# Kernel tuning notes

Measured on AMD Instinct MI355X. Metric: run time of the kernel, lower is better.

## Reference

```python
import jax, jax.numpy as jnp
import numpy as np
import math

D_MODEL = 512
H = 8
DK = D_MODEL // H  # 64
B, S = 2, 4096


def setup_inputs() -> dict:
    key = jax.random.key(0)
    ks = jax.random.split(key, 11)
    sc = 1.0 / math.sqrt(D_MODEL)
    return {
        "query": jax.random.normal(ks[0], (B, S, D_MODEL), jnp.float32),
        "key": jax.random.normal(ks[1], (B, S, D_MODEL), jnp.float32),
        "value": jax.random.normal(ks[2], (B, S, D_MODEL), jnp.float32),
        "Wq": jax.random.normal(ks[3], (D_MODEL, D_MODEL), jnp.float32) * sc,
        "bq": jnp.zeros((D_MODEL,), jnp.float32),
        "Wk": jax.random.normal(ks[4], (D_MODEL, D_MODEL), jnp.float32) * sc,
        "bk": jnp.zeros((D_MODEL,), jnp.float32),
        "Wv": jax.random.normal(ks[5], (D_MODEL, D_MODEL), jnp.float32) * sc,
        "bv": jnp.zeros((D_MODEL,), jnp.float32),
        "Wo": jax.random.normal(ks[6], (D_MODEL, D_MODEL), jnp.float32) * sc,
        "bo": jnp.zeros((D_MODEL,), jnp.float32),
    }


def reference(query, key, value, Wq, bq, Wk, bk, Wv, bv, Wo, bo):
    b = query.shape[0]
    # projections; W stored [in, out]
    def proj(x, W, bias):
        y = x @ W + bias                      # [B,S,h*dk]
        return y.reshape(b, -1, H, DK).transpose(0, 2, 1, 3)  # [B,h,S,dk]

    q = proj(query, Wq, bq)
    k = proj(key, Wk, bk)
    v = proj(value, Wv, bv)
    scores = jnp.einsum("bhqd,bhkd->bhqk", q, k) / math.sqrt(DK)
    attn = jax.nn.softmax(scores, axis=-1)    # [B,h,Sq,Sk]
    ctx = jnp.einsum("bhqk,bhkd->bhqd", attn, v)
    ctx = ctx.transpose(0, 2, 1, 3).reshape(b, -1, H * DK)  # [B,S,d_model]
    return ctx @ Wo + bo
```

## Files before the change

### kernel.cpp

```cpp
#include <hip/hip_runtime.h>
#include <hip/hip_bf16.h>

#define DM   512
#define HEADS 8
#define DKH  64
#define BATCH 2
#define SEQ  4096

typedef float  f32x4  __attribute__((ext_vector_type(4)));
typedef float  f32x16 __attribute__((ext_vector_type(16)));
typedef __bf16 bf16x8 __attribute__((ext_vector_type(8)));
typedef __bf16 bf16x4 __attribute__((ext_vector_type(4)));
typedef __bf16 bf16x2 __attribute__((ext_vector_type(2)));

static __device__ __forceinline__ f32x4 mfma16(bf16x8 a, bf16x8 b, f32x4 c) {
    return __builtin_amdgcn_mfma_f32_16x16x32_bf16(a, b, c, 0, 0, 0);
}
static __device__ __forceinline__ f32x16 mfma32(bf16x8 a, bf16x8 b, f32x16 c) {
    return __builtin_amdgcn_mfma_f32_32x32x16_bf16(a, b, c, 0, 0, 0);
}

#define GLD16(gp, lp) __builtin_amdgcn_global_load_lds( \
    (const __attribute__((address_space(1))) void*)(gp), \
    (__attribute__((address_space(3))) void*)(lp), 16, 0, 0)

struct Cvt3 { const float* s[3]; __bf16* d[3]; };

__global__ __launch_bounds__(256) void convert_x3(Cvt3 a) {
    const float* s = a.s[blockIdx.y];
    __bf16* d = a.d[blockIdx.y];
    const size_t i = ((size_t)blockIdx.x * 256 + threadIdx.x) * 8;
    f32x4 f0 = *(const f32x4*)&s[i];
    f32x4 f1 = *(const f32x4*)&s[i + 4];
    bf16x8 v;
    v[0] = (__bf16)f0[0]; v[1] = (__bf16)f0[1]; v[2] = (__bf16)f0[2]; v[3] = (__bf16)f0[3];
    v[4] = (__bf16)f1[0]; v[5] = (__bf16)f1[1]; v[6] = (__bf16)f1[2]; v[7] = (__bf16)f1[3];
    *(bf16x8*)&d[i] = v;
}

struct WtAll { const float* W[4]; __bf16* Wt[4]; };

__global__ __launch_bounds__(256) void wt_convert_all(WtAll a) {
    const float* W = a.W[blockIdx.z];
    __bf16* Wt = a.Wt[blockIdx.z];
    __shared__ float tile[32][33];
    const int tx = threadIdx.x & 31, ty = threadIdx.x >> 5;
    const int nb = blockIdx.x * 32, kb = blockIdx.y * 32;
#pragma unroll
    for (int i = 0; i < 4; ++i)
        tile[ty + 8 * i][tx] = W[(size_t)(kb + ty + 8 * i) * DM + nb + tx];
    __syncthreads();
#pragma unroll
    for (int i = 0; i < 4; ++i)
        Wt[(size_t)(nb + ty + 8 * i) * DM + kb + tx] = (__bf16)tile[tx][ty + 8 * i];
}

struct Ptr3 { const void* A; const __bf16* Bt; const float* bias; void* Out; float ascale; };
struct GemmArgs { Ptr3 p[3]; };

template <bool A_FP32, bool OUT_BF16>
__global__ __launch_bounds__(256) void gemm_tile(GemmArgs args) {
    __shared__ __bf16 Al[128][64];
    __shared__ __bf16 Bl[128][64];
    const Ptr3 P = args.p[blockIdx.z];
    const int tid = threadIdx.x;
    const int lane = tid & 63, wid = tid >> 6;
    const int lq = lane & 15, hi = lane >> 4;
    const int m0 = blockIdx.x * 128, n0 = blockIdx.y * 128;
    const int wm = (wid >> 1) * 64, wn = (wid & 1) * 64;

    const int srow = wid * 32 + (lane >> 3);
    const int scol = (lane & 7) * 8;
    const __bf16* gb = P.Bt + (size_t)(n0 + srow) * DM + scol;
    const __bf16* ga = (const __bf16*)P.A + (size_t)(m0 + srow) * DM + scol;

    f32x4 acc[4][4] = {};

    for (int kt = 0; kt < DM / 64; ++kt) {
        const int k0 = kt * 64;
        if (kt) __syncthreads();
        if (A_FP32) {
            const float* A = (const float*)P.A;
            bf16x8 abuf[4];
#pragma unroll
            for (int i = 0; i < 4; ++i) {
                int cc = tid + 256 * i, row = cc >> 3, col = cc & 7;
                const f32x4* src = (const f32x4*)&A[(size_t)(m0 + row) * DM + k0 + col * 8];
                f32x4 f0 = src[0], f1 = src[1];
                bf16x8 v;
                v[0] = (__bf16)f0[0]; v[1] = (__bf16)f0[1]; v[2] = (__bf16)f0[2]; v[3] = (__bf16)f0[3];
                v[4] = (__bf16)f1[0]; v[5] = (__bf16)f1[1]; v[6] = (__bf16)f1[2]; v[7] = (__bf16)f1[3];
                abuf[i] = v;
            }
#pragma unroll
            for (int i = 0; i < 4; ++i) {
                int cc = tid + 256 * i, row = cc >> 3, col = cc & 7;
                *(bf16x8*)&Al[row][col * 8] = abuf[i];
            }
        } else {
#pragma unroll
            for (int i = 0; i < 4; ++i)
                GLD16(ga + k0 + (size_t)i * 8 * DM, &Al[wid * 32 + i * 8][0]);
        }
#pragma unroll
        for (int i = 0; i < 4; ++i)
            GLD16(gb + k0 + (size_t)i * 8 * DM, &Bl[wid * 32 + i * 8][0]);
        __syncthreads();

        __builtin_amdgcn_s_setprio(1);
#pragma unroll
        for (int ks = 0; ks < 2; ++ks) {
            bf16x8 af[4], bfv[4];
#pragma unroll
            for (int i = 0; i < 4; ++i)
                af[i] = *(const bf16x8*)&Al[wm + i * 16 + lq][ks * 32 + hi * 8];
#pragma unroll
            for (int j = 0; j < 4; ++j)
                bfv[j] = *(const bf16x8*)&Bl[wn + j * 16 + lq][ks * 32 + hi * 8];
#pragma unroll
            for (int i = 0; i < 4; ++i)
#pragma unroll
                for (int j = 0; j < 4; ++j)
                    acc[i][j] = mfma16(af[i], bfv[j], acc[i][j]);
        }
        __builtin_amdgcn_s_setprio(0);
    }
    const float* bias = P.bias;
    const float asc = P.ascale;
#pragma unroll
    for (int j = 0; j < 4; ++j) {
        const int n = n0 + wn + j * 16 + lq;
        const float bv = bias[n];
#pragma unroll
        for (int i = 0; i < 4; ++i) {
#pragma unroll
            for (int r = 0; r < 4; ++r) {
                const int m = m0 + wm + i * 16 + hi * 4 + r;
                const float v = (acc[i][j][r] + bv) * asc;
                if (OUT_BF16) ((__bf16*)P.Out)[(size_t)m * DM + n] = (__bf16)v;
                else          ((float*)P.Out)[(size_t)m * DM + n] = v;
            }
        }
    }
}

__global__ __launch_bounds__(256) void v_transpose(const __bf16* __restrict__ Vp,
                                                   __bf16* __restrict__ Vt) {
    __shared__ __bf16 tile[64][72];
    const int tid = threadIdx.x;
    const int tt = blockIdx.x * 64;
    const int bh = blockIdx.y, b = bh >> 3, h = bh & 7;
#pragma unroll
    for (int i = 0; i < 2; ++i) {
        int c = tid + 256 * i, row = c >> 3, cc = c & 7;
        *(bf16x8*)&tile[row][cc * 8] =
            *(const bf16x8*)&Vp[(size_t)(b * SEQ + tt + row) * DM + h * DKH + cc * 8];
    }
    __syncthreads();
#pragma unroll
    for (int i = 0; i < 2; ++i) {
        int c = tid + 256 * i, row = c >> 3, cc = c & 7;
        bf16x8 v;
#pragma unroll
        for (int j = 0; j < 8; ++j) v[j] = tile[cc * 8 + j][row];
        *(bf16x8*)&Vt[(size_t)(bh * DKH + row) * SEQ + tt + cc * 8] = v;
    }
}

template <bool SPLIT>
__global__ __launch_bounds__(256, 4) void flash_attn3(const __bf16* __restrict__ Qp,
                                                      const __bf16* __restrict__ Kp,
                                                      const __bf16* __restrict__ Vt,
                                                      __bf16* __restrict__ O0,
                                                      __bf16* __restrict__ O1,
                                                      float2* __restrict__ ml) {
    __shared__ __bf16 Kl[2][64][64];
    __shared__ __bf16 Vl[2][64][64];
    __shared__ float  Lbuf[4][32];

    const int tid = threadIdx.x, lane = tid & 63, w = tid >> 6;
    const int c = lane & 31, h = lane >> 5;
    const int bh = blockIdx.y, b = bh >> 3, hd = bh & 7;
    const int qbase = blockIdx.x * 128 + w * 32;
    const int kvoff = SPLIT ? blockIdx.z * (SEQ / 2) : 0;
    const int NT = SPLIT ? (SEQ / 2) / 64 : SEQ / 64;

    bf16x8 qf[4];
#pragma unroll
    for (int t = 0; t < 4; ++t)
        qf[t] = *(const bf16x8*)&Qp[(size_t)(b * SEQ + qbase + c) * DM + hd * DKH + 16 * t + 8 * h];

    const int r0 = w * 16 + (lane >> 3);
    const int r1 = r0 + 8;
    const int s0 = (lane & 7) ^ ((r0 ^ (r0 >> 3)) & 7);
    const int s1 = (lane & 7) ^ ((r1 ^ (r1 >> 3)) & 7);
    const __bf16* kg0 = Kp + (size_t)(b * SEQ + kvoff + r0) * DM + hd * DKH + s0 * 8;
    const __bf16* kg1 = Kp + (size_t)(b * SEQ + kvoff + r1) * DM + hd * DKH + s1 * 8;
    const __bf16* vg0 = Vt + (size_t)(bh * DKH + r0) * SEQ + kvoff + s0 * 8;
    const __bf16* vg1 = Vt + (size_t)(bh * DKH + r1) * SEQ + kvoff + s1 * 8;

    const int swz0 = (c ^ (c >> 3)) & 7;
    const int swz1 = ((32 + c) ^ ((32 + c) >> 3)) & 7;
    const int rowb0 = c * 128, rowb1 = (32 + c) * 128;
    const char* kb = (const char*)&Kl[0][0][0];
    const char* vb = (const char*)&Vl[0][0][0];

    f32x16 acc0 = {}, acc1 = {};
    float m_run = -__builtin_inff(), l_run = 0.f;

    GLD16(kg0, &Kl[0][w * 16][0]);
    GLD16(kg1, &Kl[0][w * 16 + 8][0]);
    GLD16(vg0, &Vl[0][w * 16][0]);
    GLD16(vg1, &Vl[0][w * 16 + 8][0]);
    __syncthreads();

    for (int kvt = 0; kvt < NT; ++kvt) {
        const int cur = kvt & 1;
        if (kvt + 1 < NT) {
            const size_t ko = (size_t)(kvt + 1) * 64 * DM;
            const size_t vo = (size_t)(kvt + 1) * 64;
            GLD16(kg0 + ko, &Kl[cur ^ 1][w * 16][0]);
            GLD16(kg1 + ko, &Kl[cur ^ 1][w * 16 + 8][0]);
            GLD16(vg0 + vo, &Vl[cur ^ 1][w * 16][0]);
            GLD16(vg1 + vo, &Vl[cur ^ 1][w * 16 + 8][0]);
        }
        const char* kc = kb + cur * (64 * 128);
        const char* vc = vb + cur * (64 * 128);

        f32x16 sa = {}, sb = {};
        __builtin_amdgcn_s_setprio(1);
#pragma unroll
        for (int t = 0; t < 4; ++t) {
            bf16x8 kf0 = *(const bf16x8*)(kc + rowb0 + (((2 * t + h) ^ swz0) << 4));
            sa = mfma32(kf0, qf[t], sa);
            bf16x8 kf1 = *(const bf16x8*)(kc + rowb1 + (((2 * t + h) ^ swz1) << 4));
            sb = mfma32(kf1, qf[t], sb);
        }
        __builtin_amdgcn_s_setprio(0);

        float mx = sa[0];
#pragma unroll
        for (int r = 1; r < 16; ++r) mx = fmaxf(mx, sa[r]);
#pragma unroll
        for (int r = 0; r < 16; ++r) mx = fmaxf(mx, sb[r]);
        mx = fmaxf(mx, __shfl_xor(mx, 32));
        if (!__all(mx <= m_run + 8.f)) {
            const float mnew = fmaxf(m_run, mx);
            const float al = __builtin_amdgcn_exp2f(m_run - mnew);
            m_run = mnew;
            l_run *= al;
            if (lane < 32) Lbuf[w][lane] = al;
#pragma unroll
            for (int r = 0; r < 16; ++r) {
                const float a2 = Lbuf[w][(r & 3) + 8 * (r >> 2) + 4 * h];
                acc0[r] *= a2; acc1[r] *= a2;
            }
        }
        float ls = 0.f;
        float pa[16], pb[16];
#pragma unroll
        for (int r = 0; r < 16; ++r) { pa[r] = __builtin_amdgcn_exp2f(sa[r] - m_run); ls += pa[r]; }
#pragma unroll
        for (int r = 0; r < 16; ++r) { pb[r] = __builtin_amdgcn_exp2f(sb[r] - m_run); ls += pb[r]; }
        ls += __shfl_xor(ls, 32);
        l_run += ls;

        int ua[4][2], ub[4][2];
#pragma unroll
        for (int q4 = 0; q4 < 4; ++q4)
#pragma unroll
            for (int i = 0; i < 2; ++i) {
                bf16x2 ta; ta[0] = (__bf16)pa[4 * q4 + 2 * i]; ta[1] = (__bf16)pa[4 * q4 + 2 * i + 1];
                ua[q4][i] = __builtin_bit_cast(int, ta);
                bf16x2 tb; tb[0] = (__bf16)pb[4 * q4 + 2 * i]; tb[1] = (__bf16)pb[4 * q4 + 2 * i + 1];
                ub[q4][i] = __builtin_bit_cast(int, tb);
            }

#pragma unroll
        for (int tg = 0; tg < 4; ++tg) {
            int x0, y0, x1, y1;
            if (tg < 2) {
                x0 = ua[2 * tg][0]; y0 = ua[2 * tg + 1][0];
                x1 = ua[2 * tg][1]; y1 = ua[2 * tg + 1][1];
            } else {
                x0 = ub[2 * (tg - 2)][0]; y0 = ub[2 * (tg - 2) + 1][0];
                x1 = ub[2 * (tg - 2)][1]; y1 = ub[2 * (tg - 2) + 1][1];
            }
            asm("v_permlane32_swap_b32 %0, %1" : "+v"(x0), "+v"(y0));
            asm("v_permlane32_swap_b32 %0, %1" : "+v"(x1), "+v"(y1));
            union { int i4[4]; bf16x8 v; } pf;
            pf.i4[0] = x0; pf.i4[1] = x1; pf.i4[2] = y0; pf.i4[3] = y1;
            bf16x8 vf0 = *(const bf16x8*)(vc + rowb0 + (((2 * tg + h) ^ swz0) << 4));
            bf16x8 vf1 = *(const bf16x8*)(vc + rowb1 + (((2 * tg + h) ^ swz1) << 4));
            __builtin_amdgcn_s_setprio(1);
            acc0 = mfma32(pf.v, vf0, acc0);
            acc1 = mfma32(pf.v, vf1, acc1);
            __builtin_amdgcn_s_setprio(0);
        }
        __syncthreads();
    }

    if (SPLIT) {
        __bf16* pp = blockIdx.z ? O1 : O0;
#pragma unroll
        for (int r = 0; r < 16; ++r) {
            const int qr = (r & 3) + 8 * (r >> 2) + 4 * h;
            const size_t off = (size_t)(b * SEQ + qbase + qr) * DM + hd * DKH;
            pp[off + c]      = (__bf16)acc0[r];
            pp[off + 32 + c] = (__bf16)acc1[r];
        }
        if (h == 0) {
            float2 v; v.x = m_run; v.y = l_run;
            ml[(size_t)(blockIdx.z * 16 + bh) * SEQ + qbase + c] = v;
        }
    } else {
        if (lane < 32) Lbuf[w][lane] = l_run;
        __bf16* outp = O0 + (size_t)(b * SEQ + qbase) * DM + hd * DKH;
#pragma unroll
        for (int r = 0; r < 16; ++r) {
            const int qr = (r & 3) + 8 * (r >> 2) + 4 * h;
            const float li = 1.f / Lbuf[w][qr];
            outp[(size_t)qr * DM + c]      = (__bf16)(acc0[r] * li);
            outp[(size_t)qr * DM + 32 + c] = (__bf16)(acc1[r] * li);
        }
    }
}

__global__ __launch_bounds__(256) void combine(const __bf16* __restrict__ P0,
                                               const __bf16* __restrict__ P1,
                                               const float2* __restrict__ ml,
                                               __bf16* __restrict__ Ctx) {
    const int row = blockIdx.x;
    const int b = row >> 12, q = row & (SEQ - 1);
    const int col = threadIdx.x * 2;
    const int head = col >> 6;
    const int bh = b * HEADS + head;
    const float2 ml0 = ml[(size_t)bh * SEQ + q];
    const float2 ml1 = ml[(size_t)(16 + bh) * SEQ + q];
    const float m = fmaxf(ml0.x, ml1.x);
    const float e0 = __builtin_amdgcn_exp2f(ml0.x - m);
    const float e1 = __builtin_amdgcn_exp2f(ml1.x - m);
    const float inv = 1.f / (ml0.y * e0 + ml1.y * e1);
    const float f0 = e0 * inv, f1 = e1 * inv;
    const size_t idx = (size_t)row * DM + col;
    bf16x2 a = *(const bf16x2*)&P0[idx];
    bf16x2 bb = *(const bf16x2*)&P1[idx];
    bf16x2 o;
    o[0] = (__bf16)((float)a[0] * f0 + (float)bb[0] * f1);
    o[1] = (__bf16)((float)a[1] * f0 + (float)bb[1] * f1);
    *(bf16x2*)&Ctx[idx] = o;
}

extern "C" void kernel_launch(void* const* d_in, const int* in_sizes, int n_in,
                              void* d_out, int out_size, void* d_ws, size_t ws_size,
                              hipStream_t stream) {
    (void)in_sizes; (void)n_in; (void)out_size;
    const float* query = (const float*)d_in[0];
    const float* key_  = (const float*)d_in[1];
    const float* value = (const float*)d_in[2];
    const float* Wq = (const float*)d_in[3];
    const float* bq = (const float*)d_in[4];
    const float* Wk = (const float*)d_in[5];
    const float* bk = (const float*)d_in[6];
    const float* Wv = (const float*)d_in[7];
    const float* bv = (const float*)d_in[8];
    const float* Wo = (const float*)d_in[9];
    const float* bo = (const float*)d_in[10];

    char* ws = (char*)d_ws;
    const size_t WSZ = (size_t)512 * 1024;
    const size_t XSZ = (size_t)8 * 1024 * 1024;
    const float QSC = 0.125f * 1.4426950408889634f;

    __bf16* Wtq = (__bf16*)(ws);
    __bf16* Wtk = (__bf16*)(ws + WSZ);
    __bf16* Wtv = (__bf16*)(ws + 2 * WSZ);
    __bf16* Wto = (__bf16*)(ws + 3 * WSZ);
    char* xb = ws + 4 * WSZ;

    WtAll wa;
    wa.W[0] = Wq; wa.W[1] = Wk; wa.W[2] = Wv; wa.W[3] = Wo;
    wa.Wt[0] = Wtq; wa.Wt[1] = Wtk; wa.Wt[2] = Wtv; wa.Wt[3] = Wto;

    if (ws_size >= 4 * WSZ + 7 * XSZ) {
        __bf16* Qb = (__bf16*)(xb);
        __bf16* Kb = (__bf16*)(xb + XSZ);
        __bf16* Vb = (__bf16*)(xb + 2 * XSZ);
        __bf16* Qp = (__bf16*)(xb + 3 * XSZ);
        __bf16* Kp = (__bf16*)(xb + 4 * XSZ);
        __bf16* Vp = (__bf16*)(xb + 5 * XSZ);
        __bf16* Vt = (__bf16*)(xb + 6 * XSZ);
        __bf16* Ctx = Vp;
        __bf16* P0 = Qb;
        __bf16* P1 = Kb;
        float2* mlp = (float2*)Vb;

        Cvt3 cv;
        cv.s[0] = query; cv.s[1] = key_; cv.s[2] = value;
        cv.d[0] = Qb; cv.d[1] = Kb; cv.d[2] = Vb;
        convert_x3<<<dim3(2048, 3), 256, 0, stream>>>(cv);
        wt_convert_all<<<dim3(16, 16, 4), 256, 0, stream>>>(wa);

        GemmArgs qa;
        qa.p[0] = {Qb, Wtq, bq, Qp, QSC};
        qa.p[1] = {Kb, Wtk, bk, Kp, 1.0f};
        qa.p[2] = {Vb, Wtv, bv, Vp, 1.0f};
        gemm_tile<false, true><<<dim3(64, 4, 3), 256, 0, stream>>>(qa);

        v_transpose<<<dim3(SEQ / 64, BATCH * HEADS), 256, 0, stream>>>(Vp, Vt);

        flash_attn3<true><<<dim3(SEQ / 128, BATCH * HEADS, 2), 256, 0, stream>>>(
            Qp, Kp, Vt, P0, P1, mlp);

        combine<<<dim3(BATCH * SEQ), 256, 0, stream>>>(P0, P1, mlp, Ctx);

        GemmArgs oa;
        oa.p[0] = {Ctx, Wto, bo, d_out, 1.0f};
        oa.p[1] = oa.p[0]; oa.p[2] = oa.p[0];
        gemm_tile<false, false><<<dim3(64, 4, 1), 256, 0, stream>>>(oa);
    } else {
        if (ws_size < 4 * WSZ + 4 * XSZ) return;
        __bf16* Qp = (__bf16*)(xb);
        __bf16* Kp = (__bf16*)(xb + XSZ);
        __bf16* Vp = (__bf16*)(xb + 2 * XSZ);
        __bf16* Vt = (__bf16*)(xb + 3 * XSZ);
        __bf16* Ctx = Vp;

        wt_convert_all<<<dim3(16, 16, 4), 256, 0, stream>>>(wa);

        GemmArgs qa;
        qa.p[0] = {query, Wtq, bq, Qp, QSC};
        qa.p[1] = {key_,  Wtk, bk, Kp, 1.0f};
        qa.p[2] = {value, Wtv, bv, Vp, 1.0f};
        gemm_tile<true, true><<<dim3(64, 4, 3), 256, 0, stream>>>(qa);

        v_transpose<<<dim3(SEQ / 64, BATCH * HEADS), 256, 0, stream>>>(Vp, Vt);

        flash_attn3<false><<<dim3(SEQ / 128, BATCH * HEADS, 1), 256, 0, stream>>>(
            Qp, Kp, Vt, Ctx, nullptr, nullptr);

        GemmArgs oa;
        oa.p[0] = {Ctx, Wto, bo, d_out, 1.0f};
        oa.p[1] = oa.p[0]; oa.p[2] = oa.p[0];
        gemm_tile<false, false><<<dim3(64, 4, 1), 256, 0, stream>>>(oa);
    }
}
```

Baseline: 251.4 us.

## Double-buffer GEMM and attention loads, compute row sums via MFMA, swizzle GEMM LDS

The projection GEMM now double-buffers its LDS tiles with explicit vmcnt waits and raw barriers, and uses an XOR-swizzled LDS layout to avoid bank conflicts. The output GEMM switches to a 64-wide N tile so twice as many blocks are launched. The attention kernel issues the loads for tile t+2 after compute, keeping two tiles in flight. It also computes the softmax row sum with an extra MFMA against a ones vector instead of a scalar reduction and cross-lane shuffle. The fallback small-workspace path is removed, and m/l are stored as separate arrays.

```diff
diff --git a/kernel.cpp b/kernel.cpp
--- a/kernel.cpp
+++ b/kernel.cpp
@@ -10,7 +10,6 @@
 typedef float  f32x4  __attribute__((ext_vector_type(4)));
 typedef float  f32x16 __attribute__((ext_vector_type(16)));
 typedef __bf16 bf16x8 __attribute__((ext_vector_type(8)));
-typedef __bf16 bf16x4 __attribute__((ext_vector_type(4)));
 typedef __bf16 bf16x2 __attribute__((ext_vector_type(2)));
 
 static __device__ __forceinline__ f32x4 mfma16(bf16x8 a, bf16x8 b, f32x4 c) {
@@ -23,6 +22,16 @@
 #define GLD16(gp, lp) __builtin_amdgcn_global_load_lds( \
     (const __attribute__((address_space(1))) void*)(gp), \
     (__attribute__((address_space(3))) void*)(lp), 16, 0, 0)
+
+#define WAITVM(n) asm volatile("s_waitcnt vmcnt(" #n ")" ::: "memory")
+
+static __device__ __forceinline__ void barrier_sync() {
+    __builtin_amdgcn_sched_barrier(0);
+    asm volatile("" ::: "memory");
+    __builtin_amdgcn_s_barrier();
+    asm volatile("" ::: "memory");
+    __builtin_amdgcn_sched_barrier(0);
+}
 
 struct Cvt3 { const float* s[3]; __bf16* d[3]; };
 
@@ -55,80 +64,103 @@
         Wt[(size_t)(nb + ty + 8 * i) * DM + kb + tx] = (__bf16)tile[tx][ty + 8 * i];
 }
 
-struct Ptr3 { const void* A; const __bf16* Bt; const float* bias; void* Out; float ascale; };
+struct Ptr3 { const __bf16* A; const __bf16* Bt; const float* bias; void* Out; float ascale; };
 struct GemmArgs { Ptr3 p[3]; };
 
-template <bool A_FP32, bool OUT_BF16>
+template <bool OUT_BF16, int BN>
 __global__ __launch_bounds__(256) void gemm_tile(GemmArgs args) {
-    __shared__ __bf16 Al[128][64];
-    __shared__ __bf16 Bl[128][64];
+    constexpr int BGLD = BN / 32;
+    constexpr int NJ   = BN / 32;
+    constexpr int NT   = DM / 64;
+    __shared__ __bf16 Al[2][128][64];
+    __shared__ __bf16 Bl[2][BN][64];
     const Ptr3 P = args.p[blockIdx.z];
     const int tid = threadIdx.x;
     const int lane = tid & 63, wid = tid >> 6;
     const int lq = lane & 15, hi = lane >> 4;
-    const int m0 = blockIdx.x * 128, n0 = blockIdx.y * 128;
-    const int wm = (wid >> 1) * 64, wn = (wid & 1) * 64;
-
-    const int srow = wid * 32 + (lane >> 3);
-    const int scol = (lane & 7) * 8;
-    const __bf16* gb = P.Bt + (size_t)(n0 + srow) * DM + scol;
-    const __bf16* ga = (const __bf16*)P.A + (size_t)(m0 + srow) * DM + scol;
-
-    f32x4 acc[4][4] = {};
-
-    for (int kt = 0; kt < DM / 64; ++kt) {
+    const int m0 = blockIdx.x * 128, n0 = blockIdx.y * BN;
+    const int wm = (wid >> 1) * 64, wn = (wid & 1) * (BN / 2);
+
+    const int lrow = lane >> 3, lslot = lane & 7;
+    const __bf16* gaP[4];
+#pragma unroll
+    for (int i = 0; i < 4; ++i) {
+        const int r = wid * 32 + i * 8 + lrow;
+        const int s = lslot ^ ((r ^ (r >> 3)) & 7);
+        gaP[i] = P.A + (size_t)(m0 + r) * DM + s * 8;
+    }
+    const __bf16* gbP[BGLD];
+#pragma unroll
+    for (int i = 0; i < BGLD; ++i) {
+        const int r = wid * (BN / 4) + i * 8 + lrow;
+        const int s = lslot ^ ((r ^ (r >> 3)) & 7);
+        gbP[i] = P.Bt + (size_t)(n0 + r) * DM + s * 8;
+    }
+    auto stage = [&](int kt, int buf) {
         const int k0 = kt * 64;
-        if (kt) __syncthreads();
-        if (A_FP32) {
-            const float* A = (const float*)P.A;
-            bf16x8 abuf[4];
-#pragma unroll
-            for (int i = 0; i < 4; ++i) {
-                int cc = tid + 256 * i, row = cc >> 3, col = cc & 7;
-                const f32x4* src = (const f32x4*)&A[(size_t)(m0 + row) * DM + k0 + col * 8];
-                f32x4 f0 = src[0], f1 = src[1];
-                bf16x8 v;
-                v[0] = (__bf16)f0[0]; v[1] = (__bf16)f0[1]; v[2] = (__bf16)f0[2]; v[3] = (__bf16)f0[3];
-                v[4] = (__bf16)f1[0]; v[5] = (__bf16)f1[1]; v[6] = (__bf16)f1[2]; v[7] = (__bf16)f1[3];
-                abuf[i] = v;
-            }
-#pragma unroll
-            for (int i = 0; i < 4; ++i) {
-                int cc = tid + 256 * i, row = cc >> 3, col = cc & 7;
-                *(bf16x8*)&Al[row][col * 8] = abuf[i];
-            }
-        } else {
+#pragma unroll
+        for (int i = 0; i < 4; ++i)
+            GLD16(gaP[i] + k0, &Al[buf][wid * 32 + i * 8][0]);
+#pragma unroll
+        for (int i = 0; i < BGLD; ++i)
+            GLD16(gbP[i] + k0, &Bl[buf][wid * (BN / 4) + i * 8][0]);
+    };
+
+    int baseA[4], swA[4];
+#pragma unroll
+    for (int i = 0; i < 4; ++i) {
+        const int r = wm + i * 16 + lq;
+        baseA[i] = r * 128;
+        swA[i] = (((r ^ (r >> 3)) & 7) << 4);
+    }
+    int baseB[NJ], swB[NJ];
+#pragma unroll
+    for (int j = 0; j < NJ; ++j) {
+        const int r = wn + j * 16 + lq;
+        baseB[j] = r * 128;
+        swB[j] = (((r ^ (r >> 3)) & 7) << 4);
+    }
+
+    f32x4 acc[4][NJ] = {};
+
+    stage(0, 0);
+    stage(1, 1);
+    for (int kt = 0; kt < NT; ++kt) {
+        const int cur = kt & 1;
+        if (kt + 1 < NT) {
+            if (BN == 128) { WAITVM(8); } else { WAITVM(6); }
+        } else { WAITVM(0); }
+        barrier_sync();
+        const char* Ab = (const char*)&Al[cur][0][0];
+        const char* Bb = (const char*)&Bl[cur][0][0];
+        __builtin_amdgcn_s_setprio(1);
+#pragma unroll
+        for (int ks = 0; ks < 2; ++ks) {
+            const int off = ks * 64 + hi * 16;
+            bf16x8 af[4], bfv[NJ];
 #pragma unroll
             for (int i = 0; i < 4; ++i)
-                GLD16(ga + k0 + (size_t)i * 8 * DM, &Al[wid * 32 + i * 8][0]);
-        }
-#pragma unroll
-        for (int i = 0; i < 4; ++i)
-            GLD16(gb + k0 + (size_t)i * 8 * DM, &Bl[wid * 32 + i * 8][0]);
-        __syncthreads();
-
-        __builtin_amdgcn_s_setprio(1);
-#pragma unroll
-        for (int ks = 0; ks < 2; ++ks) {
-            bf16x8 af[4], bfv[4];
+                af[i] = *(const bf16x8*)(Ab + baseA[i] + (off ^ swA[i]));
+#pragma unroll
+            for (int j = 0; j < NJ; ++j)
+                bfv[j] = *(const bf16x8*)(Bb + baseB[j] + (off ^ swB[j]));
 #pragma unroll
             for (int i = 0; i < 4; ++i)
-                af[i] = *(const bf16x8*)&Al[wm + i * 16 + lq][ks * 32 + hi * 8];
-#pragma unroll
-            for (int j = 0; j < 4; ++j)
-                bfv[j] = *(const bf16x8*)&Bl[wn + j * 16 + lq][ks * 32 + hi * 8];
-#pragma unroll
-            for (int i = 0; i < 4; ++i)
-#pragma unroll
-                for (int j = 0; j < 4; ++j)
+#pragma unroll
+                for (int j = 0; j < NJ; ++j)
                     acc[i][j] = mfma16(af[i], bfv[j], acc[i][j]);
         }
         __builtin_amdgcn_s_setprio(0);
-    }
+        if (kt + 2 < NT) {
+            barrier_sync();
+            stage(kt + 2, cur);
+        }
+    }
+
     const float* bias = P.bias;
     const float asc = P.ascale;
 #pragma unroll
-    for (int j = 0; j < 4; ++j) {
+    for (int j = 0; j < NJ; ++j) {
         const int n = n0 + wn + j * 16 + lq;
         const float bv = bias[n];
 #pragma unroll
@@ -168,12 +200,13 @@
 }
 
 template <bool SPLIT>
-__global__ __launch_bounds__(256, 4) void flash_attn3(const __bf16* __restrict__ Qp,
+__global__ __launch_bounds__(256, 4) void flash_attn4(const __bf16* __restrict__ Qp,
                                                       const __bf16* __restrict__ Kp,
                                                       const __bf16* __restrict__ Vt,
                                                       __bf16* __restrict__ O0,
                                                       __bf16* __restrict__ O1,
-                                                      float2* __restrict__ ml) {
+                                                      float* __restrict__ MLM,
+                                                      float* __restrict__ MLL) {
     __shared__ __bf16 Kl[2][64][64];
     __shared__ __bf16 Vl[2][64][64];
     __shared__ float  Lbuf[4][32];
@@ -205,76 +238,83 @@
     const char* kb = (const char*)&Kl[0][0][0];
     const char* vb = (const char*)&Vl[0][0][0];
 
-    f32x16 acc0 = {}, acc1 = {};
-    float m_run = -__builtin_inff(), l_run = 0.f;
-
-    GLD16(kg0, &Kl[0][w * 16][0]);
-    GLD16(kg1, &Kl[0][w * 16 + 8][0]);
-    GLD16(vg0, &Vl[0][w * 16][0]);
-    GLD16(vg1, &Vl[0][w * 16 + 8][0]);
-    __syncthreads();
-
-    for (int kvt = 0; kvt < NT; ++kvt) {
-        const int cur = kvt & 1;
-        if (kvt + 1 < NT) {
-            const size_t ko = (size_t)(kvt + 1) * 64 * DM;
-            const size_t vo = (size_t)(kvt + 1) * 64;
-            GLD16(kg0 + ko, &Kl[cur ^ 1][w * 16][0]);
-            GLD16(kg1 + ko, &Kl[cur ^ 1][w * 16 + 8][0]);
-            GLD16(vg0 + vo, &Vl[cur ^ 1][w * 16][0]);
-            GLD16(vg1 + vo, &Vl[cur ^ 1][w * 16 + 8][0]);
-        }
-        const char* kc = kb + cur * (64 * 128);
-        const char* vc = vb + cur * (64 * 128);
+    auto stage = [&](int t, int buf) {
+        const size_t ko = (size_t)t * 64 * DM, vo = (size_t)t * 64;
+        GLD16(kg0 + ko, &Kl[buf][w * 16][0]);
+        GLD16(kg1 + ko, &Kl[buf][w * 16 + 8][0]);
+        GLD16(vg0 + vo, &Vl[buf][w * 16][0]);
+        GLD16(vg1 + vo, &Vl[buf][w * 16 + 8][0]);
+    };
+
+    bf16x8 vone;
+#pragma unroll
+    for (int j = 0; j < 8; ++j) vone[j] = (__bf16)1.0f;
+
+    f32x16 acc0 = {}, acc1 = {}, lacc = {};
+    float m_run = -__builtin_inff();
+
+    stage(0, 0);
+    stage(1, 1);
+
+    for (int t = 0; t < NT; ++t) {
+        const int cur = t & 1;
+        if (t + 1 < NT) { WAITVM(4); } else { WAITVM(0); }
+        barrier_sync();
+        const char* kc = kb + cur * 8192;
+        const char* vc = vb + cur * 8192;
 
         f32x16 sa = {}, sb = {};
         __builtin_amdgcn_s_setprio(1);
 #pragma unroll
-        for (int t = 0; t < 4; ++t) {
-            bf16x8 kf0 = *(const bf16x8*)(kc + rowb0 + (((2 * t + h) ^ swz0) << 4));
-            sa = mfma32(kf0, qf[t], sa);
-            bf16x8 kf1 = *(const bf16x8*)(kc + rowb1 + (((2 * t + h) ^ swz1) << 4));
-            sb = mfma32(kf1, qf[t], sb);
+        for (int tt = 0; tt < 4; ++tt) {
+            bf16x8 kf0 = *(const bf16x8*)(kc + rowb0 + (((2 * tt + h) ^ swz0) << 4));
+            sa = mfma32(kf0, qf[tt], sa);
+            bf16x8 kf1 = *(const bf16x8*)(kc + rowb1 + (((2 * tt + h) ^ swz1) << 4));
+            sb = mfma32(kf1, qf[tt], sb);
         }
         __builtin_amdgcn_s_setprio(0);
 
-        float mx = sa[0];
-#pragma unroll
-        for (int r = 1; r < 16; ++r) mx = fmaxf(mx, sa[r]);
-#pragma unroll
-        for (int r = 0; r < 16; ++r) mx = fmaxf(mx, sb[r]);
+        float mx = fmaxf(sa[0], sa[1]);
+#pragma unroll
+        for (int r = 2; r < 16; r += 2) mx = fmaxf(mx, fmaxf(sa[r], sa[r + 1]));
+#pragma unroll
+        for (int r = 0; r < 16; r += 2) mx = fmaxf(mx, fmaxf(sb[r], sb[r + 1]));
         mx = fmaxf(mx, __shfl_xor(mx, 32));
         if (!__all(mx <= m_run + 8.f)) {
             const float mnew = fmaxf(m_run, mx);
             const float al = __builtin_amdgcn_exp2f(m_run - mnew);
             m_run = mnew;
-            l_run *= al;
             if (lane < 32) Lbuf[w][lane] = al;
 #pragma unroll
             for (int r = 0; r < 16; ++r) {
                 const float a2 = Lbuf[w][(r & 3) + 8 * (r >> 2) + 4 * h];
-                acc0[r] *= a2; acc1[r] *= a2;
+                acc0[r] *= a2; acc1[r] *= a2; lacc[r] *= a2;
             }
         }
-        float ls = 0.f;
-        float pa[16], pb[16];
-#pragma unroll
-        for (int r = 0; r < 16; ++r) { pa[r] = __builtin_amdgcn_exp2f(sa[r] - m_run); ls += pa[r]; }
-#pragma unroll
-        for (int r = 0; r < 16; ++r) { pb[r] = __builtin_amdgcn_exp2f(sb[r] - m_run); ls += pb[r]; }
-        ls += __shfl_xor(ls, 32);
-        l_run += ls;
 
         int ua[4][2], ub[4][2];
 #pragma unroll
-        for (int q4 = 0; q4 < 4; ++q4)
-#pragma unroll
-            for (int i = 0; i < 2; ++i) {
-                bf16x2 ta; ta[0] = (__bf16)pa[4 * q4 + 2 * i]; ta[1] = (__bf16)pa[4 * q4 + 2 * i + 1];
-                ua[q4][i] = __builtin_bit_cast(int, ta);
-                bf16x2 tb; tb[0] = (__bf16)pb[4 * q4 + 2 * i]; tb[1] = (__bf16)pb[4 * q4 + 2 * i + 1];
-                ub[q4][i] = __builtin_bit_cast(int, tb);
-            }
+        for (int q4 = 0; q4 < 4; ++q4) {
+            float p0 = __builtin_amdgcn_exp2f(sa[4 * q4 + 0] - m_run);
+            float p1 = __builtin_amdgcn_exp2f(sa[4 * q4 + 1] - m_run);
+            float p2 = __builtin_amdgcn_exp2f(sa[4 * q4 + 2] - m_run);
+            float p3 = __builtin_amdgcn_exp2f(sa[4 * q4 + 3] - m_run);
+            bf16x2 t0; t0[0] = (__bf16)p0; t0[1] = (__bf16)p1;
+            bf16x2 t1; t1[0] = (__bf16)p2; t1[1] = (__bf16)p3;
+            ua[q4][0] = __builtin_bit_cast(int, t0);
+            ua[q4][1] = __builtin_bit_cast(int, t1);
+        }
+#pragma unroll
+        for (int q4 = 0; q4 < 4; ++q4) {
+            float p0 = __builtin_amdgcn_exp2f(sb[4 * q4 + 0] - m_run);
+            float p1 = __builtin_amdgcn_exp2f(sb[4 * q4 + 1] - m_run);
+            float p2 = __builtin_amdgcn_exp2f(sb[4 * q4 + 2] - m_run);
+            float p3 = __builtin_amdgcn_exp2f(sb[4 * q4 + 3] - m_run);
+            bf16x2 t0; t0[0] = (__bf16)p0; t0[1] = (__bf16)p1;
+            bf16x2 t1; t1[0] = (__bf16)p2; t1[1] = (__bf16)p3;
+            ub[q4][0] = __builtin_bit_cast(int, t0);
+            ub[q4][1] = __builtin_bit_cast(int, t1);
+        }
 
 #pragma unroll
         for (int tg = 0; tg < 4; ++tg) {
@@ -295,9 +335,14 @@
             __builtin_amdgcn_s_setprio(1);
             acc0 = mfma32(pf.v, vf0, acc0);
             acc1 = mfma32(pf.v, vf1, acc1);
+            lacc = mfma32(pf.v, vone, lacc);
             __builtin_amdgcn_s_setprio(0);
         }
-        __syncthreads();
+
+        if (t + 2 < NT) {
+            barrier_sync();
+            stage(t + 2, cur);
+        }
     }
 
     if (SPLIT) {
@@ -309,17 +354,21 @@
             pp[off + c]      = (__bf16)acc0[r];
             pp[off + 32 + c] = (__bf16)acc1[r];
         }
-        if (h == 0) {
-            float2 v; v.x = m_run; v.y = l_run;
-            ml[(size_t)(blockIdx.z * 16 + bh) * SEQ + qbase + c] = v;
+        const int zo = blockIdx.z * 16 + bh;
+        if (h == 0) MLM[(size_t)zo * SEQ + qbase + c] = m_run;
+        if (c == 0) {
+#pragma unroll
+            for (int r = 0; r < 16; ++r) {
+                const int qr = (r & 3) + 8 * (r >> 2) + 4 * h;
+                MLL[(size_t)zo * SEQ + qbase + qr] = lacc[r];
+            }
         }
     } else {
-        if (lane < 32) Lbuf[w][lane] = l_run;
         __bf16* outp = O0 + (size_t)(b * SEQ + qbase) * DM + hd * DKH;
 #pragma unroll
         for (int r = 0; r < 16; ++r) {
             const int qr = (r & 3) + 8 * (r >> 2) + 4 * h;
-            const float li = 1.f / Lbuf[w][qr];
+            const float li = 1.f / lacc[r];
             outp[(size_t)qr * DM + c]      = (__bf16)(acc0[r] * li);
             outp[(size_t)qr * DM + 32 + c] = (__bf16)(acc1[r] * li);
         }
@@ -328,19 +377,22 @@
 
 __global__ __launch_bounds__(256) void combine(const __bf16* __restrict__ P0,
                                                const __bf16* __restrict__ P1,
-                                               const float2* __restrict__ ml,
+                                               const float* __restrict__ MLM,
+                                               const float* __restrict__ MLL,
                                                __bf16* __restrict__ Ctx) {
     const int row = blockIdx.x;
     const int b = row >> 12, q = row & (SEQ - 1);
     const int col = threadIdx.x * 2;
     const int head = col >> 6;
     const int bh = b * HEADS + head;
-    const float2 ml0 = ml[(size_t)bh * SEQ + q];
-    const float2 ml1 = ml[(size_t)(16 + bh) * SEQ + q];
-    const float m = fmaxf(ml0.x, ml1.x);
-    const float e0 = __builtin_amdgcn_exp2f(ml0.x - m);
-    const float e1 = __builtin_amdgcn_exp2f(ml1.x - m);
-    const float inv = 1.f / (ml0.y * e0 + ml1.y * e1);
+    const float m0 = MLM[(size_t)bh * SEQ + q];
+    const float m1 = MLM[(size_t)(16 + bh) * SEQ + q];
+    const float l0 = MLL[(size_t)bh * SEQ + q];
+    const float l1 = MLL[(size_t)(16 + bh) * SEQ + q];
+    const float m = fmaxf(m0, m1);
+    const float e0 = __builtin_amdgcn_exp2f(m0 - m);
+    const float e1 = __builtin_amdgcn_exp2f(m1 - m);
+    const float inv = 1.f / (l0 * e0 + l1 * e1);
     const float f0 = e0 * inv, f1 = e1 * inv;
     const size_t idx = (size_t)row * DM + col;
     bf16x2 a = *(const bf16x2*)&P0[idx];
@@ -371,77 +423,51 @@
     const size_t WSZ = (size_t)512 * 1024;
     const size_t XSZ = (size_t)8 * 1024 * 1024;
     const float QSC = 0.125f * 1.4426950408889634f;
+    if (ws_size < 4 * WSZ + 7 * XSZ) return;
 
     __bf16* Wtq = (__bf16*)(ws);
     __bf16* Wtk = (__bf16*)(ws + WSZ);
     __bf16* Wtv = (__bf16*)(ws + 2 * WSZ);
     __bf16* Wto = (__bf16*)(ws + 3 * WSZ);
     char* xb = ws + 4 * WSZ;
+    __bf16* Qb = (__bf16*)(xb);
+    __bf16* Kb = (__bf16*)(xb + XSZ);
+    __bf16* Vb = (__bf16*)(xb + 2 * XSZ);
+    __bf16* Qp = (__bf16*)(xb + 3 * XSZ);
+    __bf16* Kp = (__bf16*)(xb + 4 * XSZ);
+    __bf16* Vp = (__bf16*)(xb + 5 * XSZ);
+    __bf16* Vt = (__bf16*)(xb + 6 * XSZ);
+    __bf16* Ctx = Vp;
+    __bf16* P0 = Qb;
+    __bf16* P1 = Kb;
+    float* MLM = (float*)Vb;
+    float* MLL = MLM + 2 * 16 * SEQ;
+
+    Cvt3 cv;
+    cv.s[0] = query; cv.s[1] = key_; cv.s[2] = value;
+    cv.d[0] = Qb; cv.d[1] = Kb; cv.d[2] = Vb;
+    convert_x3<<<dim3(2048, 3), 256, 0, stream>>>(cv);
 
     WtAll wa;
     wa.W[0] = Wq; wa.W[1] = Wk; wa.W[2] = Wv; wa.W[3] = Wo;
     wa.Wt[0] = Wtq; wa.Wt[1] = Wtk; wa.Wt[2] = Wtv; wa.Wt[3] = Wto;
-
-    if (ws_size >= 4 * WSZ + 7 * XSZ) {
-        __bf16* Qb = (__bf16*)(xb);
-        __bf16* Kb = (__bf16*)(xb + XSZ);
-        __bf16* Vb = (__bf16*)(xb + 2 * XSZ);
-        __bf16* Qp = (__bf16*)(xb + 3 * XSZ);
-        __bf16* Kp = (__bf16*)(xb + 4 * XSZ);
-        __bf16* Vp = (__bf16*)(xb + 5 * XSZ);
-        __bf16* Vt = (__bf16*)(xb + 6 * XSZ);
-        __bf16* Ctx = Vp;
-        __bf16* P0 = Qb;
-        __bf16* P1 = Kb;
-        float2* mlp = (float2*)Vb;
-
-        Cvt3 cv;
-        cv.s[0] = query; cv.s[1] = key_; cv.s[2] = value;
-        cv.d[0] = Qb; cv.d[1] = Kb; cv.d[2] = Vb;
-        convert_x3<<<dim3(2048, 3), 256, 0, stream>>>(cv);
-        wt_convert_all<<<dim3(16, 16, 4), 256, 0, stream>>>(wa);
-
-        GemmArgs qa;
-        qa.p[0] = {Qb, Wtq, bq, Qp, QSC};
-        qa.p[1] = {Kb, Wtk, bk, Kp, 1.0f};
-        qa.p[2] = {Vb, Wtv, bv, Vp, 1.0f};
-        gemm_tile<false, true><<<dim3(64, 4, 3), 256, 0, stream>>>(qa);
-
-        v_transpose<<<dim3(SEQ / 64, BATCH * HEADS), 256, 0, stream>>>(Vp, Vt);
-
-        flash_attn3<true><<<dim3(SEQ / 128, BATCH * HEADS, 2), 256, 0, stream>>>(
-            Qp, Kp, Vt, P0, P1, mlp);
-
-        combine<<<dim3(BATCH * SEQ), 256, 0, stream>>>(P0, P1, mlp, Ctx);
-
-        GemmArgs oa;
-        oa.p[0] = {Ctx, Wto, bo, d_out, 1.0f};
-        oa.p[1] = oa.p[0]; oa.p[2] = oa.p[0];
-        gemm_tile<false, false><<<dim3(64, 4, 1), 256, 0, stream>>>(oa);
-    } else {
-        if (ws_size < 4 * WSZ + 4 * XSZ) return;
-        __bf16* Qp = (__bf16*)(xb);
-        __bf16* Kp = (__bf16*)(xb + XSZ);
-        __bf16* Vp = (__bf16*)(xb + 2 * XSZ);
-        __bf16* Vt = (__bf16*)(xb + 3 * XSZ);
-        __bf16* Ctx = Vp;
-
-        wt_convert_all<<<dim3(16, 16, 4), 256, 0, stream>>>(wa);
-
-        GemmArgs qa;
-        qa.p[0] = {query, Wtq, bq, Qp, QSC};
-        qa.p[1] = {key_,  Wtk, bk, Kp, 1.0f};
-        qa.p[2] = {value, Wtv, bv, Vp, 1.0f};
-        gemm_tile<true, true><<<dim3(64, 4, 3), 256, 0, stream>>>(qa);
-
-        v_transpose<<<dim3(SEQ / 64, BATCH * HEADS), 256, 0, stream>>>(Vp, Vt);
-
-        flash_attn3<false><<<dim3(SEQ / 128, BATCH * HEADS, 1), 256, 0, stream>>>(
-            Qp, Kp, Vt, Ctx, nullptr, nullptr);
-
-        GemmArgs oa;
-        oa.p[0] = {Ctx, Wto, bo, d_out, 1.0f};
-        oa.p[1] = oa.p[0]; oa.p[2] = oa.p[0];
-        gemm_tile<false, false><<<dim3(64, 4, 1), 256, 0, stream>>>(oa);
-    }
-}
+    wt_convert_all<<<dim3(16, 16, 4), 256, 0, stream>>>(wa);
+
+    GemmArgs qa;
+    qa.p[0] = {Qb, Wtq, bq, Qp, QSC};
+    qa.p[1] = {Kb, Wtk, bk, Kp, 1.0f};
+    qa.p[2] = {Vb, Wtv, bv, Vp, 1.0f};
+    gemm_tile<true, 128><<<dim3(64, 4, 3), 256, 0, stream>>>(qa);
+
+    v_transpose<<<dim3(SEQ / 64, BATCH * HEADS), 256, 0, stream>>>(Vp, Vt);
+
+    flash_attn4<true><<<dim3(SEQ / 128, BATCH * HEADS, 2), 256, 0, stream>>>(
+        Qp, Kp, Vt, P0, P1, MLM, MLL);
+
+    combine<<<dim3(BATCH * SEQ), 256, 0, stream>>>(P0, P1, MLM, MLL, Ctx);
+
+    GemmArgs oa;
+    oa.p[0] = {Ctx, Wto, bo, d_out, 1.0f};
+    oa.p[1] = oa.p[0]; oa.p[2] = oa.p[0];
+    gemm_tile<false, 64><<<dim3(64, 8, 1), 256, 0, stream>>>(oa);
+}
```

Result: slower. 266.9 us (+6.1%).
